# Kernel optimization log

Measured on AMD Instinct MI355X. Metric: run time of the kernel, lower is better.

Reference implementation:

```python
import jax, jax.numpy as jnp
import numpy as np

B, L, K, D = 16, 2048, 24, 64  # batch, seq_len (input_len), num_eigh, d_out (= d_in)


def _hankel_eigh(l, k):
    # Hankel matrix Z[i,j] = 2 / ((i+j)^3 - (i+j)), 1-indexed (spectral filtering of LDS)
    s = np.arange(1, l + 1, dtype=np.int64)[:, None] + np.arange(1, l + 1, dtype=np.int64)[None, :]
    z = 2.0 / (s.astype(np.float64) ** 3 - s.astype(np.float64))
    ev, evec = np.linalg.eigh(z)
    # top-k eigenpairs (eigh returns ascending order)
    return jnp.asarray(ev[-k:], jnp.float32), jnp.asarray(evec[:, -k:], jnp.float32)


def setup_inputs() -> dict:
    key = jax.random.key(0)
    k1, k2 = jax.random.split(key)
    inputs = jax.random.normal(k1, (B, L, D), dtype=jnp.float32)
    m_phi = jax.random.normal(k2, (D * K, D), dtype=jnp.float32) / np.float32(np.sqrt(D * K))
    eig_vals, eig_vecs = _hankel_eigh(L, K)  # [K], [L, K]
    return {"inputs": inputs, "m_phi": m_phi, "eig_vals": eig_vals, "eig_vecs": eig_vecs}


def _compute_x_tilde(inputs, eig_vals, eig_vecs):
    # Causal FFT convolution of each Hankel eigenvector (filter, length L) with input.
    l = inputs.shape[1]
    n = 2 * l  # fft length >= 2l - 1 for linear (non-circular) convolution
    V = jnp.fft.rfft(eig_vecs, n=n, axis=0)            # [F, K]
    U = jnp.fft.rfft(inputs, n=n, axis=1)              # [B, F, D]
    prod = V[None, :, :, None] * U[:, :, None, :]      # [B, F, K, D]
    x = jnp.fft.irfft(prod, n=n, axis=1)[:, :l]        # truncate to causal part: [B, L, K, D]
    x = x * (eig_vals ** 0.25)[None, None, :, None]    # spectral scaling
    return x.reshape(x.shape[0], l, -1)                # [B, L, K*D]


def reference(inputs, m_phi, eig_vals, eig_vecs):
    x_tilde = _compute_x_tilde(inputs, eig_vals, eig_vecs)
    return x_tilde @ m_phi  # delta_phi: [B, L, D]
```

## Files before the change

kernel.cpp:

```cpp
#include <hip/hip_runtime.h>

typedef _Float16 f16;
typedef _Float16 f16x4 __attribute__((ext_vector_type(4)));
typedef _Float16 f16x8 __attribute__((ext_vector_type(8)));
typedef float f32x4 __attribute__((ext_vector_type(4)));

__device__ __forceinline__ void gl_lds16(const void* g, void* l) {
  __builtin_amdgcn_global_load_lds(
      (__attribute__((address_space(1))) unsigned int*)(g),
      (__attribute__((address_space(3))) unsigned int*)(l), 16, 0, 0);
}

__global__ __launch_bounds__(256) void k_pre0(const float* __restrict__ in,
                                              const float* __restrict__ m_phi,
                                              const float* __restrict__ ev,
                                              const float* __restrict__ evec,
                                              f16* __restrict__ phiT,
                                              f16* __restrict__ uin,
                                              f16* __restrict__ Dpre,
                                              float* __restrict__ out) {
  __shared__ float esm[256];
  int blk = blockIdx.x;
  int tid = threadIdx.x;
  if (blk < 256) {
    int b = blk >> 4, s0 = (blk & 15) * 128;
    f16* up = uin + (size_t)blk * 8192;
#pragma unroll
    for (int v = 0; v < 4; ++v) {
      int flat = v * 256 + tid;
      int row = flat >> 3, cl = flat & 7, cg = cl ^ (row & 7);
      const float* g = in + ((size_t)(b * 2048 + s0 + row)) * 64 + cg * 8;
      float4 u0 = *(const float4*)g;
      float4 u1 = *(const float4*)(g + 4);
      f16x8 h;
      h[0] = (f16)u0.x; h[1] = (f16)u0.y; h[2] = (f16)u0.z; h[3] = (f16)u0.w;
      h[4] = (f16)u1.x; h[5] = (f16)u1.y; h[6] = (f16)u1.z; h[7] = (f16)u1.w;
      *(f16x8*)&up[flat * 8] = h;
    }
    return;
  }
  if (blk < 280) {
    int k = blk - 256;
    for (int idx = tid; idx < 4096; idx += 256) {
      int e = idx >> 6, d = idx & 63;
      phiT[k * 4096 + idx] = (f16)m_phi[(k * 64 + d) * 64 + e];
    }
    return;
  }
  if (blk < 664) {
    int a = blk - 280;
    int diag = a / 24, k = a % 24;
    float s4 = sqrtf(sqrtf(ev[k]));
    int base = diag * 128 - 127;
    if (tid < 255) {
      int v = base + tid;
      esm[tid] = (v >= 0) ? evec[v * 24 + k] * s4 : 0.0f;
    }
    __syncthreads();
    f16* plane = Dpre + (size_t)(diag * 24 + k) * 2560;
    for (int i = tid; i < 2560; i += 256) {
      float val = 0.f;
      if (i < 2112) {
        int p = i / 264, y = i - p * 264;
        int g = 254 - p - y;
        if (g >= 0) val = esm[g];
      }
      plane[i] = (f16)val;
    }
    return;
  }
  float4* o = (float4*)(out + (size_t)(blk - 664) * 32768);
  float4 z4 = {0.f, 0.f, 0.f, 0.f};
#pragma unroll
  for (int i = 0; i < 32; ++i) o[i * 256 + tid] = z4;
}

__global__ __launch_bounds__(256) void k_w(const f16* __restrict__ uin,
                                           const f16* __restrict__ phiT,
                                           f16* __restrict__ W2T) {
  __shared__ __align__(16) f16 Ubuf[8320];
  __shared__ __align__(16) f16 Psm[64 * 64];
  int wblk = blockIdx.x;
  int s0 = (wblk & 15) * 128;
  int b = (wblk >> 4) & 15;
  int kg = wblk >> 8;
  int tid = threadIdx.x, lane = tid & 63, wv = tid >> 6;
  const f16* up = uin + (size_t)(wblk & 255) * 8192;
#pragma unroll
  for (int v = 0; v < 4; ++v)
    gl_lds16(up + (size_t)(v * 256 + tid) * 8, &Ubuf[(v * 256 + wv * 64) * 8]);
  {
    int k0 = kg * 4;
#pragma unroll
    for (int v = 0; v < 2; ++v) {
      int flat = v * 256 + tid;
      int row = flat >> 3, cl = flat & 7, cg = cl ^ (row & 7);
      gl_lds16(phiT + (size_t)k0 * 4096 + row * 64 + cg * 8,
               &Psm[(v * 256 + wv * 64) * 8]);
    }
  }
  __syncthreads();
  int wm = wv * 32;
  f16x8 af[2][2];
#pragma unroll
  for (int ks = 0; ks < 2; ++ks)
#pragma unroll
    for (int x = 0; x < 2; ++x) {
      int m = wm + x * 16 + (lane & 15);
      int ch = (ks * 4 + (lane >> 4)) ^ (m & 7);
      af[ks][x] = *(const f16x8*)&Ubuf[m * 64 + ch * 8];
    }
  for (int ki = 0; ki < 4; ++ki) {
    int k = kg * 4 + ki;
    f32x4 zero = {0.f, 0.f, 0.f, 0.f};
    f32x4 acc[2][4];
#pragma unroll
    for (int x = 0; x < 2; ++x)
#pragma unroll
      for (int y = 0; y < 4; ++y) acc[x][y] = zero;
#pragma unroll
    for (int ks = 0; ks < 2; ++ks) {
      f16x8 bf[4];
#pragma unroll
      for (int y = 0; y < 4; ++y) {
        int n = y * 16 + (lane & 15);
        int ch = (ks * 4 + (lane >> 4)) ^ (n & 7);
        bf[y] = *(const f16x8*)&Psm[n * 64 + ch * 8];
      }
#pragma unroll
      for (int x = 0; x < 2; ++x)
#pragma unroll
        for (int y = 0; y < 4; ++y)
          acc[x][y] = __builtin_amdgcn_mfma_f32_16x16x32_f16(af[ks][x], bf[y], acc[x][y], 0, 0, 0);
    }
    __syncthreads();
#pragma unroll
    for (int x = 0; x < 2; ++x)
#pragma unroll
      for (int y = 0; y < 4; ++y) {
        int e = y * 16 + (lane & 15);
        int sg = wm + x * 16 + ((lane >> 4) << 2);
        f16x4 pk;
        pk[0] = (f16)acc[x][y][0]; pk[1] = (f16)acc[x][y][1];
        pk[2] = (f16)acc[x][y][2]; pk[3] = (f16)acc[x][y][3];
        *(f16x4*)&Ubuf[e * 130 + sg] = pk;
      }
    if (ki < 3) {
      int kn = k + 1;
#pragma unroll
      for (int v = 0; v < 2; ++v) {
        int flat = v * 256 + tid;
        int row = flat >> 3, cl = flat & 7, cg = cl ^ (row & 7);
        gl_lds16(phiT + (size_t)kn * 4096 + row * 64 + cg * 8,
                 &Psm[(v * 256 + wv * 64) * 8]);
      }
    }
    __syncthreads();
#pragma unroll
    for (int pass = 0; pass < 4; ++pass) {
      int g = pass * 256 + tid;
      int e = g >> 4, ch = g & 15;
      f16x8 val = *(const f16x8*)&Ubuf[e * 130 + ch * 8];
      *(f16x8*)&W2T[((size_t)((b * 24 + k) * 64 + e)) * 2048 + s0 + ch * 8] = val;
    }
  }
}

__global__ __launch_bounds__(256, 3) void k_main(const f16* __restrict__ Dpre,
                                                 const f16* __restrict__ W2T,
                                                 float* __restrict__ out) {
  __shared__ __align__(16) f16 Bsm[128 * 128];
  __shared__ __align__(16) f16 Dsm[2560];
  int nt = blockIdx.x;
  int q = blockIdx.y;
  int diag = 0, off = 0;
  while (off + (16 - diag) <= q) { off += 16 - diag; ++diag; }
  int st = q - off;
  int mt = st + diag;
  int tid = threadIdx.x, lane = tid & 63, wv = tid >> 6;
  int wm = (wv & 1) * 64, wn = (wv >> 1) * 64;
  int b0 = nt * 2;
  int ml = lane & 15, qv = lane >> 4;
  int p264 = (7 - (ml & 7)) * 264;
  int yb = (ml < 8 ? 120 : 112) - wm;

  f32x4 zero = {0.f, 0.f, 0.f, 0.f};
  f32x4 acc[4][4];
#pragma unroll
  for (int x = 0; x < 4; ++x)
#pragma unroll
    for (int y = 0; y < 4; ++y) acc[x][y] = zero;

  const f16* dplane = Dpre + (size_t)(diag * 24) * 2560;

  for (int k = 0; k < 24; ++k) {
    const f16* dk = dplane + k * 2560;
    gl_lds16(dk + tid * 8, &Dsm[(wv * 64) * 8]);
    if (wv == 0) gl_lds16(dk + (256 + lane) * 8, &Dsm[2048]);
#pragma unroll
    for (int v = 0; v < 8; ++v) {
      int flat = v * 256 + tid;
      int row = flat >> 4, cl = flat & 15, cg = cl ^ (row & 15);
      int bb = b0 + (row >> 6), e = row & 63;
      gl_lds16(W2T + ((size_t)((bb * 24 + k) * 64 + e)) * 2048 + st * 128 + cg * 8,
               &Bsm[(v * 256 + wv * 64) * 8]);
    }
    __syncthreads();
#pragma unroll
    for (int ks = 0; ks < 4; ++ks) {
      int s0q = ks * 32 + qv * 8;
      f16x8 af[4], bf[4];
#pragma unroll
      for (int x = 0; x < 4; ++x)
        af[x] = *(const f16x8*)&Dsm[p264 + s0q - x * 16 + yb];
#pragma unroll
      for (int y = 0; y < 4; ++y) {
        int n = wn + y * 16 + ml;
        int cl = (ks * 4 + qv) ^ (n & 15);
        bf[y] = *(const f16x8*)&Bsm[n * 128 + cl * 8];
      }
#pragma unroll
      for (int x = 0; x < 4; ++x)
#pragma unroll
        for (int y = 0; y < 4; ++y)
          acc[x][y] = __builtin_amdgcn_mfma_f32_16x16x32_f16(af[x], bf[y], acc[x][y], 0, 0, 0);
    }
    __syncthreads();
  }
  int t0 = mt * 128 + wm;
  int n0 = nt * 128 + wn;
#pragma unroll
  for (int x = 0; x < 4; ++x) {
    int rbase = t0 + x * 16 + (qv << 2);
#pragma unroll
    for (int y = 0; y < 4; ++y) {
      int col = n0 + y * 16 + ml;
      int b = col >> 6, e = col & 63;
#pragma unroll
      for (int r = 0; r < 4; ++r)
        atomicAdd(&out[((size_t)(b * 2048 + rbase + r)) * 64 + e], acc[x][y][r]);
    }
  }
}

extern "C" void kernel_launch(void* const* d_in, const int* in_sizes, int n_in,
                              void* d_out, int out_size, void* d_ws, size_t ws_size,
                              hipStream_t stream) {
  const float* inputs = (const float*)d_in[0];
  const float* m_phi = (const float*)d_in[1];
  const float* ev = (const float*)d_in[2];
  const float* evec = (const float*)d_in[3];
  float* out = (float*)d_out;
  char* ws = (char*)d_ws;
  f16* Dpre = (f16*)(ws);
  f16* phiT = (f16*)(ws + 1966080);
  f16* uin = (f16*)(ws + 2162688);
  f16* W2T = (f16*)(ws + 6356992);

  hipLaunchKernelGGL(k_pre0, dim3(728), dim3(256), 0, stream,
                     inputs, m_phi, ev, evec, phiT, uin, Dpre, out);
  hipLaunchKernelGGL(k_w, dim3(1536), dim3(256), 0, stream, uin, phiT, W2T);
  hipLaunchKernelGGL(k_main, dim3(8, 136), dim3(256), 0, stream, Dpre, W2T, out);
}
```

Baseline: 214.7 us.

## Fuse input-projection GEMM into main Toeplitz GEMM, dropping W2T round trip

Removes the separate k_w kernel that wrote the projected inputs (U·phi_k) to a large global W2T buffer. Each k_main2 block now computes its 128x128 W tile per k on the fly from uin and phiT held in LDS, then feeds it to the Toeplitz-diagonal MFMA. This avoids a kernel launch and a large global write and read-back. In exchange, the projection is recomputed once per diagonal block (redundant MFMA work), LDS use grows, and occupancy is lowered to 2 blocks per SM.

```diff
diff --git a/kernel.cpp b/kernel.cpp
--- a/kernel.cpp
+++ b/kernel.cpp
@@ -75,102 +75,14 @@
   for (int i = 0; i < 32; ++i) o[i * 256 + tid] = z4;
 }
 
-__global__ __launch_bounds__(256) void k_w(const f16* __restrict__ uin,
-                                           const f16* __restrict__ phiT,
-                                           f16* __restrict__ W2T) {
-  __shared__ __align__(16) f16 Ubuf[8320];
-  __shared__ __align__(16) f16 Psm[64 * 64];
-  int wblk = blockIdx.x;
-  int s0 = (wblk & 15) * 128;
-  int b = (wblk >> 4) & 15;
-  int kg = wblk >> 8;
-  int tid = threadIdx.x, lane = tid & 63, wv = tid >> 6;
-  const f16* up = uin + (size_t)(wblk & 255) * 8192;
-#pragma unroll
-  for (int v = 0; v < 4; ++v)
-    gl_lds16(up + (size_t)(v * 256 + tid) * 8, &Ubuf[(v * 256 + wv * 64) * 8]);
-  {
-    int k0 = kg * 4;
-#pragma unroll
-    for (int v = 0; v < 2; ++v) {
-      int flat = v * 256 + tid;
-      int row = flat >> 3, cl = flat & 7, cg = cl ^ (row & 7);
-      gl_lds16(phiT + (size_t)k0 * 4096 + row * 64 + cg * 8,
-               &Psm[(v * 256 + wv * 64) * 8]);
-    }
-  }
-  __syncthreads();
-  int wm = wv * 32;
-  f16x8 af[2][2];
-#pragma unroll
-  for (int ks = 0; ks < 2; ++ks)
-#pragma unroll
-    for (int x = 0; x < 2; ++x) {
-      int m = wm + x * 16 + (lane & 15);
-      int ch = (ks * 4 + (lane >> 4)) ^ (m & 7);
-      af[ks][x] = *(const f16x8*)&Ubuf[m * 64 + ch * 8];
-    }
-  for (int ki = 0; ki < 4; ++ki) {
-    int k = kg * 4 + ki;
-    f32x4 zero = {0.f, 0.f, 0.f, 0.f};
-    f32x4 acc[2][4];
-#pragma unroll
-    for (int x = 0; x < 2; ++x)
-#pragma unroll
-      for (int y = 0; y < 4; ++y) acc[x][y] = zero;
-#pragma unroll
-    for (int ks = 0; ks < 2; ++ks) {
-      f16x8 bf[4];
-#pragma unroll
-      for (int y = 0; y < 4; ++y) {
-        int n = y * 16 + (lane & 15);
-        int ch = (ks * 4 + (lane >> 4)) ^ (n & 7);
-        bf[y] = *(const f16x8*)&Psm[n * 64 + ch * 8];
-      }
-#pragma unroll
-      for (int x = 0; x < 2; ++x)
-#pragma unroll
-        for (int y = 0; y < 4; ++y)
-          acc[x][y] = __builtin_amdgcn_mfma_f32_16x16x32_f16(af[ks][x], bf[y], acc[x][y], 0, 0, 0);
-    }
-    __syncthreads();
-#pragma unroll
-    for (int x = 0; x < 2; ++x)
-#pragma unroll
-      for (int y = 0; y < 4; ++y) {
-        int e = y * 16 + (lane & 15);
-        int sg = wm + x * 16 + ((lane >> 4) << 2);
-        f16x4 pk;
-        pk[0] = (f16)acc[x][y][0]; pk[1] = (f16)acc[x][y][1];
-        pk[2] = (f16)acc[x][y][2]; pk[3] = (f16)acc[x][y][3];
-        *(f16x4*)&Ubuf[e * 130 + sg] = pk;
-      }
-    if (ki < 3) {
-      int kn = k + 1;
-#pragma unroll
-      for (int v = 0; v < 2; ++v) {
-        int flat = v * 256 + tid;
-        int row = flat >> 3, cl = flat & 7, cg = cl ^ (row & 7);
-        gl_lds16(phiT + (size_t)kn * 4096 + row * 64 + cg * 8,
-                 &Psm[(v * 256 + wv * 64) * 8]);
-      }
-    }
-    __syncthreads();
-#pragma unroll
-    for (int pass = 0; pass < 4; ++pass) {
-      int g = pass * 256 + tid;
-      int e = g >> 4, ch = g & 15;
-      f16x8 val = *(const f16x8*)&Ubuf[e * 130 + ch * 8];
-      *(f16x8*)&W2T[((size_t)((b * 24 + k) * 64 + e)) * 2048 + s0 + ch * 8] = val;
-    }
-  }
-}
-
-__global__ __launch_bounds__(256, 3) void k_main(const f16* __restrict__ Dpre,
-                                                 const f16* __restrict__ W2T,
-                                                 float* __restrict__ out) {
-  __shared__ __align__(16) f16 Bsm[128 * 128];
+__global__ __launch_bounds__(256, 2) void k_main2(const f16* __restrict__ Dpre,
+                                                  const f16* __restrict__ phiT,
+                                                  const f16* __restrict__ uin,
+                                                  float* __restrict__ out) {
+  __shared__ __align__(16) f16 Ubuf[2 * 8192];
+  __shared__ __align__(16) f16 Psm[4096];
   __shared__ __align__(16) f16 Dsm[2560];
+  __shared__ __align__(16) f16 Bsm[16384];
   int nt = blockIdx.x;
   int q = blockIdx.y;
   int diag = 0, off = 0;
@@ -178,11 +90,13 @@
   int st = q - off;
   int mt = st + diag;
   int tid = threadIdx.x, lane = tid & 63, wv = tid >> 6;
+  int ml = lane & 15, qv = lane >> 4;
   int wm = (wv & 1) * 64, wn = (wv >> 1) * 64;
   int b0 = nt * 2;
-  int ml = lane & 15, qv = lane >> 4;
   int p264 = (7 - (ml & 7)) * 264;
   int yb = (ml < 8 ? 120 : 112) - wm;
+  int bb = wv >> 1;
+  int sh = (wv & 1) * 64;
 
   f32x4 zero = {0.f, 0.f, 0.f, 0.f};
   f32x4 acc[4][4];
@@ -191,19 +105,76 @@
 #pragma unroll
     for (int y = 0; y < 4; ++y) acc[x][y] = zero;
 
+  const f16* up0 = uin + (size_t)(b0 * 16 + st) * 8192;
+  const f16* up1 = uin + (size_t)((b0 + 1) * 16 + st) * 8192;
+#pragma unroll
+  for (int v = 0; v < 4; ++v)
+    gl_lds16(up0 + (size_t)(v * 256 + tid) * 8, &Ubuf[(v * 256 + wv * 64) * 8]);
+#pragma unroll
+  for (int v = 0; v < 4; ++v)
+    gl_lds16(up1 + (size_t)(v * 256 + tid) * 8, &Ubuf[8192 + (v * 256 + wv * 64) * 8]);
+#pragma unroll
+  for (int v = 0; v < 2; ++v) {
+    int flat = v * 256 + tid;
+    int row = flat >> 3, cl = flat & 7, cg = cl ^ (row & 7);
+    gl_lds16(phiT + row * 64 + cg * 8, &Psm[(v * 256 + wv * 64) * 8]);
+  }
+  __syncthreads();
+
   const f16* dplane = Dpre + (size_t)(diag * 24) * 2560;
+  const f16* ub = Ubuf + bb * 8192;
 
   for (int k = 0; k < 24; ++k) {
+    f32x4 accw[4][4];
+#pragma unroll
+    for (int x = 0; x < 4; ++x)
+#pragma unroll
+      for (int y = 0; y < 4; ++y) accw[x][y] = zero;
+#pragma unroll
+    for (int ks = 0; ks < 2; ++ks) {
+      f16x8 afw[4], bfw[4];
+#pragma unroll
+      for (int x = 0; x < 4; ++x) {
+        int s = sh + x * 16 + ml;
+        int ch = (ks * 4 + qv) ^ (s & 7);
+        afw[x] = *(const f16x8*)&ub[s * 64 + ch * 8];
+      }
+#pragma unroll
+      for (int y = 0; y < 4; ++y) {
+        int e = y * 16 + ml;
+        int ch = (ks * 4 + qv) ^ (e & 7);
+        bfw[y] = *(const f16x8*)&Psm[e * 64 + ch * 8];
+      }
+#pragma unroll
+      for (int x = 0; x < 4; ++x)
+#pragma unroll
+        for (int y = 0; y < 4; ++y)
+          accw[x][y] = __builtin_amdgcn_mfma_f32_16x16x32_f16(afw[x], bfw[y], accw[x][y], 0, 0, 0);
+    }
+    __syncthreads();
     const f16* dk = dplane + k * 2560;
     gl_lds16(dk + tid * 8, &Dsm[(wv * 64) * 8]);
     if (wv == 0) gl_lds16(dk + (256 + lane) * 8, &Dsm[2048]);
 #pragma unroll
-    for (int v = 0; v < 8; ++v) {
+    for (int x = 0; x < 4; ++x) {
+      int s_loc = sh + x * 16 + qv * 4;
+      int c = s_loc >> 3, so = s_loc & 7;
+#pragma unroll
+      for (int y = 0; y < 4; ++y) {
+        int n = bb * 64 + y * 16 + ml;
+        f16x4 pk;
+        pk[0] = (f16)accw[x][y][0]; pk[1] = (f16)accw[x][y][1];
+        pk[2] = (f16)accw[x][y][2]; pk[3] = (f16)accw[x][y][3];
+        *(f16x4*)&Bsm[n * 128 + (c ^ (n & 15)) * 8 + so] = pk;
+      }
+    }
+    int kn = (k < 23) ? k + 1 : 23;
+#pragma unroll
+    for (int v = 0; v < 2; ++v) {
       int flat = v * 256 + tid;
-      int row = flat >> 4, cl = flat & 15, cg = cl ^ (row & 15);
-      int bb = b0 + (row >> 6), e = row & 63;
-      gl_lds16(W2T + ((size_t)((bb * 24 + k) * 64 + e)) * 2048 + st * 128 + cg * 8,
-               &Bsm[(v * 256 + wv * 64) * 8]);
+      int row = flat >> 3, cl = flat & 7, cg = cl ^ (row & 7);
+      gl_lds16(phiT + (size_t)kn * 4096 + row * 64 + cg * 8,
+               &Psm[(v * 256 + wv * 64) * 8]);
     }
     __syncthreads();
 #pragma unroll
@@ -225,7 +196,6 @@
         for (int y = 0; y < 4; ++y)
           acc[x][y] = __builtin_amdgcn_mfma_f32_16x16x32_f16(af[x], bf[y], acc[x][y], 0, 0, 0);
     }
-    __syncthreads();
   }
   int t0 = mt * 128 + wm;
   int n0 = nt * 128 + wn;
@@ -255,10 +225,9 @@
   f16* Dpre = (f16*)(ws);
   f16* phiT = (f16*)(ws + 1966080);
   f16* uin = (f16*)(ws + 2162688);
-  f16* W2T = (f16*)(ws + 6356992);
 
   hipLaunchKernelGGL(k_pre0, dim3(728), dim3(256), 0, stream,
                      inputs, m_phi, ev, evec, phiT, uin, Dpre, out);
-  hipLaunchKernelGGL(k_w, dim3(1536), dim3(256), 0, stream, uin, phiT, W2T);
-  hipLaunchKernelGGL(k_main, dim3(8, 136), dim3(256), 0, stream, Dpre, W2T, out);
-}
+  hipLaunchKernelGGL(k_main2, dim3(8, 136), dim3(256), 0, stream,
+                     Dpre, phiT, uin, out);
+}
```

After: 231.3 us. +7.7%, slower.
